# Kernel tuning notes

Hardware: AMD Instinct MI355X
Metric: run time of the kernel (lower is better)

## Reference

```python
import jax, jax.numpy as jnp
import numpy as np

NUM_BINS = 10
NUM_CLASSES = 128
ALPHA = 0.999
LABEL_SMOOTHING = 0.0


def setup_inputs() -> dict:
    key = jax.random.key(0)
    k1, k2, k3 = jax.random.split(key, 3)
    B, T, C = 16, 4096, NUM_CLASSES
    return {
        "pred_logits": jax.random.normal(k1, (B, T, C), dtype=jnp.float32),
        "target_prob": jax.random.uniform(k2, (B, T, C), dtype=jnp.float32),
        "mask": jax.random.uniform(k3, (B, T, 1), dtype=jnp.float32),
        "GD_stat_ema": jnp.ones((NUM_BINS,), dtype=jnp.float32),
        "label_stat_ema_each_class": jnp.ones((NUM_CLASSES * 3,), dtype=jnp.float32),
    }


def _bce_with_logits(x, t):
    # numerically stable BCEWithLogitsLoss, reduction='none'
    return jnp.maximum(x, 0.0) - x * t + jnp.log1p(jnp.exp(-jnp.abs(x)))


def _update_ema(ema, hist, num_bins):
    hist = hist / jnp.maximum(hist.sum(), 1e-10) * num_bins
    ema = ema * ALPHA + (1.0 - ALPHA) * hist
    return ema / jnp.maximum(ema.sum(), 1e-10) * num_bins


def reference(pred_logits, target_prob, mask, GD_stat_ema, label_stat_ema_each_class):
    m = jnp.broadcast_to(mask, pred_logits.shape)
    tp = jnp.clip(target_prob, LABEL_SMOOTHING, 1.0 - LABEL_SMOOTHING)

    raw_loss = _bce_with_logits(pred_logits, tp)
    pred_prob = jax.nn.sigmoid(pred_logits)
    grad_mag = jnp.abs(pred_prob - tp)

    bin_idx = jnp.clip(jnp.floor(grad_mag * NUM_BINS).astype(jnp.int32), 0, NUM_BINS - 1)
    GD_weights = 1.0 / jax.lax.stop_gradient(GD_stat_ema[bin_idx])

    # per-class 3-way probability bin: idx in [0, 3*num_classes)
    tpi = jnp.clip(jnp.floor(tp * 3.0).astype(jnp.int32), 0, 2) + 3 * jnp.arange(NUM_CLASSES, dtype=jnp.int32)
    classes_weights = 1.0 / jax.lax.stop_gradient(label_stat_ema_each_class[tpi])

    weights = jnp.sqrt(GD_weights * classes_weights)
    loss = (raw_loss * weights * m).sum() / jnp.maximum(m.sum(), 1e-10)

    # weighted histograms (bincount with float weights)
    GD_hist = jnp.zeros((NUM_BINS,), dtype=jnp.float32).at[bin_idx.ravel()].add(m.ravel())
    label_hist = jnp.zeros((NUM_CLASSES * 3,), dtype=jnp.float32).at[tpi.ravel()].add(m.ravel())

    GD_ema_new = _update_ema(GD_stat_ema, GD_hist, NUM_BINS)
    label_ema_new = _update_ema(label_stat_ema_each_class, label_hist, NUM_CLASSES * 3)
    return loss, GD_ema_new, label_ema_new
```

## Files before the change

### kernel.cpp

```cpp
#include <hip/hip_runtime.h>

#define NBINS 10
#define NCLS  128
#define LBINS 384
#define NSLICE 8
#define SLICE_STRIDE 512
#define GRID 2048
#define BLOCK 256
#define ITER 4
#define GSTRIDE (GRID * BLOCK)

__global__ __launch_bounds__(256, 3) void ghm_main(
    const float* __restrict__ xg, const float* __restrict__ tg,
    const float* __restrict__ mask,
    const float* __restrict__ gd_ema, const float* __restrict__ lab_ema,
    float* __restrict__ ws)
{
    __shared__ float s_rsgd[NBINS];
    __shared__ float s_rslab[LBINS];
    __shared__ float s_hlab[LBINS];
    __shared__ float s_hgd[NBINS];
    __shared__ float s_red[4];

    const int tid = threadIdx.x;
    if (tid < NBINS) { s_rsgd[tid] = __builtin_amdgcn_rsqf(gd_ema[tid]); s_hgd[tid] = 0.f; }
    for (int i = tid; i < LBINS; i += BLOCK) {
        s_rslab[i] = __builtin_amdgcn_rsqf(lab_ema[i]);
        s_hlab[i]  = 0.f;
    }
    __syncthreads();

    const int c0 = (tid & 31) * 4;
    float wl[4][3];
#pragma unroll
    for (int j = 0; j < 4; ++j)
#pragma unroll
        for (int t = 0; t < 3; ++t) wl[j][t] = s_rslab[(c0 + j) * 3 + t];

    float lab[4][3] = {{0.f}};
    float gdl[NBINS];
#pragma unroll
    for (int b = 0; b < NBINS; ++b) gdl[b] = 0.f;
    float loss_acc = 0.f;

    const float4* x4 = (const float4*)xg;
    const float4* t4 = (const float4*)tg;
    const int i0 = blockIdx.x * BLOCK + tid;

    float4 xv[ITER], tv[ITER]; float mv[ITER];
#pragma unroll
    for (int k = 0; k < ITER; ++k) {
        const int i = i0 + k * GSTRIDE;
        xv[k] = x4[i];
        tv[k] = t4[i];
        mv[k] = mask[i >> 5];
    }

#pragma unroll
    for (int k = 0; k < ITER; ++k) {
        const float m = mv[k];
        const float xs[4] = {xv[k].x, xv[k].y, xv[k].z, xv[k].w};
        const float ts[4] = {tv[k].x, tv[k].y, tv[k].z, tv[k].w};
        unsigned pack = 0u;
#pragma unroll
        for (int j = 0; j < 4; ++j) {
            const float x  = xs[j];
            const float tp = ts[j];
            const float E  = __expf(-fabsf(x));
            const float z  = 1.f + E;
            const float raw = fmaxf(x, 0.f) - x * tp + __logf(z);
            const float inv = __builtin_amdgcn_rcpf(z);
            const float tps = (x >= 0.f) ? tp : 1.f - tp;
            const float g   = fabsf(inv - tps);
            int bin = (int)(g * 10.f);  bin = bin > 9 ? 9 : bin;
            int t3  = (int)(tp * 3.f);  t3  = t3 > 2 ? 2 : t3;
            const float wlj = (t3 == 0) ? wl[j][0] : ((t3 == 1) ? wl[j][1] : wl[j][2]);
            const float w = s_rsgd[bin] * wlj;
            loss_acc = fmaf(raw * m, w, loss_acc);
#pragma unroll
            for (int t = 0; t < 3; ++t) lab[j][t] += (t3 == t) ? m : 0.f;
            pack += 1u << (3 * bin);
        }
#pragma unroll
        for (int b = 0; b < NBINS; ++b)
            gdl[b] = fmaf(m, (float)((pack >> (3 * b)) & 7u), gdl[b]);
    }

    const int lane = tid & 63, wv = tid >> 6;
    float v = loss_acc;
#pragma unroll
    for (int off = 32; off > 0; off >>= 1) v += __shfl_down(v, off);
    if (lane == 0) s_red[wv] = v;

#pragma unroll
    for (int b = 0; b < NBINS; ++b) {
        float g = gdl[b];
#pragma unroll
        for (int off = 32; off > 0; off >>= 1) g += __shfl_down(g, off);
        if (lane == 0) atomicAdd(&s_hgd[b], g);
    }
#pragma unroll
    for (int j = 0; j < 4; ++j)
#pragma unroll
        for (int t = 0; t < 3; ++t)
            atomicAdd(&s_hlab[(c0 + j) * 3 + t], lab[j][t]);
    __syncthreads();

    float* wss = ws + (blockIdx.x & (NSLICE - 1)) * SLICE_STRIDE;
    if (tid == 0) atomicAdd(&wss[0], s_red[0] + s_red[1] + s_red[2] + s_red[3]);
    if (tid < NBINS) atomicAdd(&wss[1 + tid], s_hgd[tid]);
    for (int e = tid; e < LBINS; e += BLOCK) atomicAdd(&wss[1 + NBINS + e], s_hlab[e]);
}

__global__ __launch_bounds__(512) void ghm_fin(
    const float* __restrict__ ws,
    const float* __restrict__ gd_ema, const float* __restrict__ lab_ema,
    float* __restrict__ out)
{
    __shared__ float red[512];
    __shared__ float s_gde[NBINS];
    __shared__ float s_gesum;

    const int tid = threadIdx.x;

    float v = 0.f;
    if (tid < 1 + NBINS + LBINS) {
#pragma unroll
        for (int s = 0; s < NSLICE; ++s) v += ws[s * SLICE_STRIDE + tid];
    }

    red[tid] = (tid >= 1 && tid < 1 + NBINS) ? v : 0.f;
    __syncthreads();
    for (int off = 256; off > 0; off >>= 1) {
        if (tid < off) red[tid] += red[tid + off];
        __syncthreads();
    }
    const float msum = red[0];
    __syncthreads();
    const float inv_m = 1.f / fmaxf(msum, 1e-10f);

    if (tid == 0) out[0] = v * inv_m;

    if (tid >= 1 && tid < 1 + NBINS) {
        float hn = v * inv_m * (float)NBINS;
        s_gde[tid - 1] = gd_ema[tid - 1] * 0.999f + 0.001f * hn;
    }
    __syncthreads();
    if (tid == 0) {
        float s = 0.f;
        for (int b = 0; b < NBINS; ++b) s += s_gde[b];
        s_gesum = s;
    }
    __syncthreads();
    if (tid >= 1 && tid < 1 + NBINS)
        out[tid] = s_gde[tid - 1] / fmaxf(s_gesum, 1e-10f) * (float)NBINS;

    float e = 0.f;
    if (tid >= 1 + NBINS && tid < 1 + NBINS + LBINS) {
        float hn = v * inv_m * (float)LBINS;
        e = lab_ema[tid - 1 - NBINS] * 0.999f + 0.001f * hn;
    }
    red[tid] = e;
    __syncthreads();
    for (int off = 256; off > 0; off >>= 1) {
        if (tid < off) red[tid] += red[tid + off];
        __syncthreads();
    }
    const float esum = red[0];
    if (tid >= 1 + NBINS && tid < 1 + NBINS + LBINS)
        out[tid] = e / fmaxf(esum, 1e-10f) * (float)LBINS;
}

extern "C" void kernel_launch(void* const* d_in, const int* in_sizes, int n_in,
                              void* d_out, int out_size, void* d_ws, size_t ws_size,
                              hipStream_t stream)
{
    const float* logits  = (const float*)d_in[0];
    const float* tprob   = (const float*)d_in[1];
    const float* mask    = (const float*)d_in[2];
    const float* gd_ema  = (const float*)d_in[3];
    const float* lab_ema = (const float*)d_in[4];
    float* out = (float*)d_out;
    float* ws  = (float*)d_ws;

    hipMemsetAsync(ws, 0, NSLICE * SLICE_STRIDE * sizeof(float), stream);
    ghm_main<<<GRID, BLOCK, 0, stream>>>(logits, tprob, mask, gd_ema, lab_ema, ws);
    ghm_fin<<<1, 512, 0, stream>>>(ws, gd_ema, lab_ema, out);
}
```

Before: 145.7 us.

## Replace global atomics and memset with per-block partial slots reduced in finalizer

A new path has each of 1024 blocks write its loss, GD histogram and label histogram partials to its own workspace slot with plain stores, instead of doing global atomics into 8 slices. That removes the memset launch and the contention on global atomics. The finalizer then reduces all 1024 slots with float4 loads. Each block also processes 8 float4 per thread in two batches of four instead of four per thread over 2048 blocks. The old atomic path stays as a fallback when the workspace is too small, and the finalizer now has more serial reduction work to do.

```diff
diff --git a/kernel.cpp b/kernel.cpp
--- a/kernel.cpp
+++ b/kernel.cpp
@@ -1,16 +1,186 @@
 #include <hip/hip_runtime.h>
 
 #define NBINS 10
-#define NCLS  128
 #define LBINS 384
+#define NOUT  395
+#define PSTRIDE 400
+#define BLOCK 256
+
+#define SGRID 1024
+#define OUTER 2
+#define BATCH 4
+#define SGSTR (SGRID * BLOCK)
+
+__global__ __launch_bounds__(256) void ghm_main_s(
+    const float* __restrict__ xg, const float* __restrict__ tg,
+    const float* __restrict__ mask,
+    const float* __restrict__ gd_ema, const float* __restrict__ lab_ema,
+    float* __restrict__ ws)
+{
+    __shared__ float s_rsgd[NBINS];
+    __shared__ float s_rslab[LBINS];
+    __shared__ float s_out[PSTRIDE];
+    __shared__ float s_red[4];
+
+    const int tid = threadIdx.x;
+    if (tid < NBINS) s_rsgd[tid] = __builtin_amdgcn_rsqf(gd_ema[tid]);
+    for (int i = tid; i < LBINS; i += BLOCK) s_rslab[i] = __builtin_amdgcn_rsqf(lab_ema[i]);
+    for (int i = tid; i < PSTRIDE; i += BLOCK) s_out[i] = 0.f;
+    __syncthreads();
+
+    const int c0 = (tid & 31) * 4;
+    float wl[4][3];
+#pragma unroll
+    for (int j = 0; j < 4; ++j)
+#pragma unroll
+        for (int t = 0; t < 3; ++t) wl[j][t] = s_rslab[(c0 + j) * 3 + t];
+
+    float lab[4][3] = {{0.f}};
+    float gdl[NBINS];
+#pragma unroll
+    for (int b = 0; b < NBINS; ++b) gdl[b] = 0.f;
+    float loss_acc = 0.f;
+
+    const float4* x4 = (const float4*)xg;
+    const float4* t4 = (const float4*)tg;
+    const int i0 = blockIdx.x * BLOCK + tid;
+
+#pragma unroll
+    for (int o = 0; o < OUTER; ++o) {
+        float4 xv[BATCH], tv[BATCH]; float mv[BATCH];
+#pragma unroll
+        for (int k = 0; k < BATCH; ++k) {
+            const int i = i0 + (o * BATCH + k) * SGSTR;
+            xv[k] = x4[i];
+            tv[k] = t4[i];
+            mv[k] = mask[i >> 5];
+        }
+#pragma unroll
+        for (int k = 0; k < BATCH; ++k) {
+            const float m = mv[k];
+            const float xs[4] = {xv[k].x, xv[k].y, xv[k].z, xv[k].w};
+            const float ts[4] = {tv[k].x, tv[k].y, tv[k].z, tv[k].w};
+            unsigned pack = 0u;
+#pragma unroll
+            for (int j = 0; j < 4; ++j) {
+                const float x  = xs[j];
+                const float tp = ts[j];
+                const float E  = __expf(-fabsf(x));
+                const float z  = 1.f + E;
+                const float raw = fmaxf(x, 0.f) - x * tp + __logf(z);
+                const float inv = __builtin_amdgcn_rcpf(z);
+                const float tps = (x >= 0.f) ? tp : 1.f - tp;
+                const float g   = fabsf(inv - tps);
+                int bin = (int)(g * 10.f);  bin = bin > 9 ? 9 : bin;
+                int t3  = (int)(tp * 3.f);  t3  = t3 > 2 ? 2 : t3;
+                const float wlj = (t3 == 0) ? wl[j][0] : ((t3 == 1) ? wl[j][1] : wl[j][2]);
+                const float w = s_rsgd[bin] * wlj;
+                loss_acc = fmaf(raw * m, w, loss_acc);
+#pragma unroll
+                for (int t = 0; t < 3; ++t) lab[j][t] += (t3 == t) ? m : 0.f;
+                pack += 1u << (3 * bin);
+            }
+#pragma unroll
+            for (int b = 0; b < NBINS; ++b)
+                gdl[b] = fmaf(m, (float)((pack >> (3 * b)) & 7u), gdl[b]);
+        }
+    }
+
+    const int lane = tid & 63, wv = tid >> 6;
+    float v = loss_acc;
+#pragma unroll
+    for (int off = 32; off > 0; off >>= 1) v += __shfl_down(v, off);
+    if (lane == 0) s_red[wv] = v;
+#pragma unroll
+    for (int b = 0; b < NBINS; ++b) {
+        float g = gdl[b];
+#pragma unroll
+        for (int off = 32; off > 0; off >>= 1) g += __shfl_down(g, off);
+        if (lane == 0) atomicAdd(&s_out[1 + b], g);
+    }
+#pragma unroll
+    for (int j = 0; j < 4; ++j)
+#pragma unroll
+        for (int t = 0; t < 3; ++t)
+            atomicAdd(&s_out[11 + (c0 + j) * 3 + t], lab[j][t]);
+    __syncthreads();
+
+    float* slot = ws + (size_t)blockIdx.x * PSTRIDE;
+    if (tid == 0) slot[0] = s_red[0] + s_red[1] + s_red[2] + s_red[3];
+    if (tid >= 1) slot[tid] = s_out[tid];
+    if (tid < PSTRIDE - BLOCK) slot[BLOCK + tid] = s_out[BLOCK + tid];
+}
+
+__global__ __launch_bounds__(512) void ghm_fin_s(
+    const float* __restrict__ ws,
+    const float* __restrict__ gd_ema, const float* __restrict__ lab_ema,
+    float* __restrict__ out)
+{
+    __shared__ float4 s4[512];
+    __shared__ float  sv[PSTRIDE];
+    __shared__ float  red[512];
+    __shared__ float  s_sc[1];
+
+    const int tid = threadIdx.x;
+    const int sub = tid >> 7, q = tid & 127;
+
+    float ax = 0.f, ay = 0.f, az = 0.f, aw = 0.f;
+    if (q < PSTRIDE / 4) {
+        const float4* p = (const float4*)ws + q;
+#pragma unroll 4
+        for (int b = sub; b < SGRID; b += 4) {
+            float4 u = p[b * (PSTRIDE / 4)];
+            ax += u.x; ay += u.y; az += u.z; aw += u.w;
+        }
+    }
+    s4[tid] = make_float4(ax, ay, az, aw);
+    __syncthreads();
+    if (tid < PSTRIDE / 4) {
+        float4 a = s4[tid], b4 = s4[tid + 128], c = s4[tid + 256], d = s4[tid + 384];
+        sv[4 * tid + 0] = a.x + b4.x + c.x + d.x;
+        sv[4 * tid + 1] = a.y + b4.y + c.y + d.y;
+        sv[4 * tid + 2] = a.z + b4.z + c.z + d.z;
+        sv[4 * tid + 3] = a.w + b4.w + c.w + d.w;
+    }
+    __syncthreads();
+
+    if (tid == 0) {
+        float ms = 0.f;
+        for (int b = 0; b < NBINS; ++b) ms += sv[1 + b];
+        const float inv_m = 1.f / fmaxf(ms, 1e-10f);
+        s_sc[0] = inv_m;
+        out[0] = sv[0] * inv_m;
+        float ge[NBINS], gs = 0.f;
+        for (int b = 0; b < NBINS; ++b) {
+            ge[b] = gd_ema[b] * 0.999f + 0.001f * (sv[1 + b] * inv_m * (float)NBINS);
+            gs += ge[b];
+        }
+        const float ig = 1.f / fmaxf(gs, 1e-10f);
+        for (int b = 0; b < NBINS; ++b) out[1 + b] = ge[b] * ig * (float)NBINS;
+    }
+    __syncthreads();
+    const float inv_m = s_sc[0];
+
+    float e = 0.f;
+    if (tid < LBINS)
+        e = lab_ema[tid] * 0.999f + 0.001f * (sv[11 + tid] * inv_m * (float)LBINS);
+    red[tid] = e;
+    __syncthreads();
+    for (int off = 256; off > 0; off >>= 1) {
+        if (tid < off) red[tid] += red[tid + off];
+        __syncthreads();
+    }
+    const float ie = (float)LBINS / fmaxf(red[0], 1e-10f);
+    if (tid < LBINS) out[11 + tid] = e * ie;
+}
+
 #define NSLICE 8
 #define SLICE_STRIDE 512
-#define GRID 2048
-#define BLOCK 256
-#define ITER 4
-#define GSTRIDE (GRID * BLOCK)
-
-__global__ __launch_bounds__(256, 3) void ghm_main(
+#define AGRID 2048
+#define AITER 4
+#define AGSTR (AGRID * BLOCK)
+
+__global__ __launch_bounds__(256, 3) void ghm_main_a(
     const float* __restrict__ xg, const float* __restrict__ tg,
     const float* __restrict__ mask,
     const float* __restrict__ gd_ema, const float* __restrict__ lab_ema,
@@ -47,17 +217,14 @@
     const float4* t4 = (const float4*)tg;
     const int i0 = blockIdx.x * BLOCK + tid;
 
-    float4 xv[ITER], tv[ITER]; float mv[ITER];
-#pragma unroll
-    for (int k = 0; k < ITER; ++k) {
-        const int i = i0 + k * GSTRIDE;
-        xv[k] = x4[i];
-        tv[k] = t4[i];
-        mv[k] = mask[i >> 5];
-    }
-
-#pragma unroll
-    for (int k = 0; k < ITER; ++k) {
+    float4 xv[AITER], tv[AITER]; float mv[AITER];
+#pragma unroll
+    for (int k = 0; k < AITER; ++k) {
+        const int i = i0 + k * AGSTR;
+        xv[k] = x4[i]; tv[k] = t4[i]; mv[k] = mask[i >> 5];
+    }
+#pragma unroll
+    for (int k = 0; k < AITER; ++k) {
         const float m = mv[k];
         const float xs[4] = {xv[k].x, xv[k].y, xv[k].z, xv[k].w};
         const float ts[4] = {tv[k].x, tv[k].y, tv[k].z, tv[k].w};
@@ -91,7 +258,6 @@
 #pragma unroll
     for (int off = 32; off > 0; off >>= 1) v += __shfl_down(v, off);
     if (lane == 0) s_red[wv] = v;
-
 #pragma unroll
     for (int b = 0; b < NBINS; ++b) {
         float g = gdl[b];
@@ -112,7 +278,7 @@
     for (int e = tid; e < LBINS; e += BLOCK) atomicAdd(&wss[1 + NBINS + e], s_hlab[e]);
 }
 
-__global__ __launch_bounds__(512) void ghm_fin(
+__global__ __launch_bounds__(512) void ghm_fin_a(
     const float* __restrict__ ws,
     const float* __restrict__ gd_ema, const float* __restrict__ lab_ema,
     float* __restrict__ out)
@@ -122,13 +288,11 @@
     __shared__ float s_gesum;
 
     const int tid = threadIdx.x;
-
     float v = 0.f;
-    if (tid < 1 + NBINS + LBINS) {
+    if (tid < NOUT) {
 #pragma unroll
         for (int s = 0; s < NSLICE; ++s) v += ws[s * SLICE_STRIDE + tid];
     }
-
     red[tid] = (tid >= 1 && tid < 1 + NBINS) ? v : 0.f;
     __syncthreads();
     for (int off = 256; off > 0; off >>= 1) {
@@ -138,9 +302,7 @@
     const float msum = red[0];
     __syncthreads();
     const float inv_m = 1.f / fmaxf(msum, 1e-10f);
-
     if (tid == 0) out[0] = v * inv_m;
-
     if (tid >= 1 && tid < 1 + NBINS) {
         float hn = v * inv_m * (float)NBINS;
         s_gde[tid - 1] = gd_ema[tid - 1] * 0.999f + 0.001f * hn;
@@ -156,7 +318,7 @@
         out[tid] = s_gde[tid - 1] / fmaxf(s_gesum, 1e-10f) * (float)NBINS;
 
     float e = 0.f;
-    if (tid >= 1 + NBINS && tid < 1 + NBINS + LBINS) {
+    if (tid >= 1 + NBINS && tid < NOUT) {
         float hn = v * inv_m * (float)LBINS;
         e = lab_ema[tid - 1 - NBINS] * 0.999f + 0.001f * hn;
     }
@@ -167,7 +329,7 @@
         __syncthreads();
     }
     const float esum = red[0];
-    if (tid >= 1 + NBINS && tid < 1 + NBINS + LBINS)
+    if (tid >= 1 + NBINS && tid < NOUT)
         out[tid] = e / fmaxf(esum, 1e-10f) * (float)LBINS;
 }
 
@@ -183,7 +345,13 @@
     float* out = (float*)d_out;
     float* ws  = (float*)d_ws;
 
-    hipMemsetAsync(ws, 0, NSLICE * SLICE_STRIDE * sizeof(float), stream);
-    ghm_main<<<GRID, BLOCK, 0, stream>>>(logits, tprob, mask, gd_ema, lab_ema, ws);
-    ghm_fin<<<1, 512, 0, stream>>>(ws, gd_ema, lab_ema, out);
-}
+    const size_t need = (size_t)SGRID * PSTRIDE * sizeof(float);
+    if (ws_size >= need) {
+        ghm_main_s<<<SGRID, BLOCK, 0, stream>>>(logits, tprob, mask, gd_ema, lab_ema, ws);
+        ghm_fin_s<<<1, 512, 0, stream>>>(ws, gd_ema, lab_ema, out);
+    } else {
+        hipMemsetAsync(ws, 0, NSLICE * SLICE_STRIDE * sizeof(float), stream);
+        ghm_main_a<<<AGRID, BLOCK, 0, stream>>>(logits, tprob, mask, gd_ema, lab_ema, ws);
+        ghm_fin_a<<<1, 512, 0, stream>>>(ws, gd_ema, lab_ema, out);
+    }
+}
```

After: 153.9 us. +5.6%, slower.
